# Kernel tuning notes

Measured on AMD Instinct MI355X. Metric: run time of the kernel, lower is better.

## Reference

```python
import jax, jax.numpy as jnp
import numpy as np

B, S, T = 32, 128, 64
H = 512
VS = VT = 32000


def _lstm_cell(x, h, c, W, U, b):
    # Keras LSTM gate order: i, f, g(cell), o
    z = x @ W + h @ U + b
    i, f, g, o = jnp.split(z, 4, axis=-1)
    c = jax.nn.sigmoid(f) * c + jax.nn.sigmoid(i) * jnp.tanh(g)
    h = jax.nn.sigmoid(o) * jnp.tanh(c)
    return h, c


def _lstm_scan(xs, h0, c0, W, U, b):
    # xs: [S, B, D]
    def step(carry, x):
        h, c = _lstm_cell(x, carry[0], carry[1], W, U, b)
        return (h, c), h
    (hT, cT), hs = jax.lax.scan(step, (h0, c0), xs)
    return hs, hT, cT


def setup_inputs() -> dict:
    key = jax.random.key(0)
    ks = jax.random.split(key, 16)
    def n(k, shape, s=0.02):
        return (jax.random.normal(k, shape, jnp.float32) * s).astype(jnp.float32)
    return {
        "src": jax.random.randint(ks[0], (B, S), 0, VS, jnp.int32),
        "trg": jax.random.randint(ks[1], (B, T), 0, VT, jnp.int32),
        "E_src": n(ks[2], (VS, H)),
        "E_trg": n(ks[3], (VT, H)),
        "Wf": n(ks[4], (H, 4 * H)), "Uf": n(ks[5], (H, 4 * H)), "bf": jnp.zeros((4 * H,), jnp.float32),
        "Wb": n(ks[6], (H, 4 * H)), "Ub": n(ks[7], (H, 4 * H)), "bb": jnp.zeros((4 * H,), jnp.float32),
        "Wd": n(ks[8], (H, 4 * H)), "Ud": n(ks[9], (H, 4 * H)), "bd": jnp.zeros((4 * H,), jnp.float32),
        "fcW": n(ks[10], (2 * H, H)), "fcb": jnp.zeros((H,), jnp.float32),
        "clsW": n(ks[11], (2 * H, VT)), "clsb": jnp.zeros((VT,), jnp.float32),
    }


def reference(src, trg, E_src, E_trg, Wf, Uf, bf, Wb, Ub, bb, Wd, Ud, bd, fcW, fcb, clsW, clsb):
    Bn = src.shape[0]
    Hn = E_src.shape[1]
    # --- Encoder: bidirectional LSTM ---
    xs = E_src[src].transpose(1, 0, 2)          # [S, B, H]
    z0 = jnp.zeros((Bn, Hn), xs.dtype)
    hs_f, hf, cf = _lstm_scan(xs, z0, z0, Wf, Uf, bf)
    hs_b, hb, cb = _lstm_scan(xs[::-1], z0, z0, Wb, Ub, bb)
    src_hidden = jnp.concatenate([hs_f, hs_b[::-1]], axis=-1).transpose(1, 0, 2)  # [B, S, 2H]
    # --- shared fc projections (same Dense, 2H -> H) ---
    src_h = src_hidden @ fcW + fcb                                   # [B, S, H]
    prev_h = jnp.concatenate([hf, hb], axis=-1) @ fcW + fcb          # [B, H]
    prev_c = jnp.concatenate([cf, cb], axis=-1) @ fcW + fcb          # [B, H]
    neg = jnp.where(src == 0, jnp.float32(-1e9), jnp.float32(0.0))   # [B, S]
    # --- Decoder (teacher forcing): per-step LSTM cell + dot-product attention ---
    ys = E_trg[trg[:, :-1]].transpose(1, 0, 2)  # [T-1, B, H]

    def step(carry, x):
        h, c = _lstm_cell(x, carry[0], carry[1], Wd, Ud, bd)
        score = jnp.einsum('bh,bsh->bs', h, src_h) + neg
        attn = jax.nn.softmax(score, axis=-1)
        ws = jnp.einsum('bs,bsh->bh', attn, src_h)
        return (h, c), jnp.concatenate([ws, h], axis=-1)  # dec_state [B, 2H]

    _, dec = jax.lax.scan(step, (prev_h, prev_c), ys)     # [T-1, B, 2H]
    logits = dec.transpose(1, 0, 2) @ clsW + clsb          # [B, T-1, VT]
    return logits
```

## Files before the change

### kernel.cpp

```cpp
#include <hip/hip_runtime.h>
#include <hip/hip_bf16.h>
#include <stdint.h>
#include <string.h>

constexpr int cB = 32, cS = 128, cT = 64, cH = 512, cH4 = 2048, cVT = 32000, cTM1 = 63;

typedef __attribute__((ext_vector_type(8))) __bf16 bf16x8;
typedef __attribute__((ext_vector_type(4))) float f32x4;

__device__ __forceinline__ float sigm(float x) { return 1.0f / (1.0f + expf(-x)); }

__device__ __forceinline__ bf16x8 sc_load16(const __hip_bfloat16* p) {
  bf16x8 r;
  asm volatile("global_load_dwordx4 %0, %1, off sc0 sc1"
               : "=&v"(r) : "v"(p) : "memory");
  return r;
}
__device__ __forceinline__ void sc_store2(__hip_bfloat16* p, float hval) {
  __hip_bfloat16 hb = __float2bfloat16(hval);
  unsigned short us;
  memcpy(&us, &hb, 2);
  unsigned u = us;
  asm volatile("global_store_short %0, %1, off sc0 sc1"
               :: "v"(p), "v"(u) : "memory");
}

__device__ __forceinline__ void gridbar(unsigned* ctr, unsigned* flag,
                                        unsigned nblk, unsigned gen) {
  asm volatile("s_waitcnt vmcnt(0)" ::: "memory");
  __syncthreads();
  if (threadIdx.x == 0) {
    unsigned old = __hip_atomic_fetch_add(ctr, 1u, __ATOMIC_RELAXED,
                                          __HIP_MEMORY_SCOPE_AGENT);
    if (old == gen * nblk - 1u) {
      __hip_atomic_store(flag, gen, __ATOMIC_RELAXED, __HIP_MEMORY_SCOPE_AGENT);
    } else {
      while (__hip_atomic_load(flag, __ATOMIC_RELAXED, __HIP_MEMORY_SCOPE_AGENT) < gen)
        __builtin_amdgcn_s_sleep(1);
    }
  }
  __syncthreads();
}

__global__ __launch_bounds__(64) void k_init_bars(unsigned* p) {
  if (threadIdx.x < 16) p[threadIdx.x] = 0u;
}

__global__ __launch_bounds__(128) void k_embed_src(const int* __restrict__ src,
                                                   const float* __restrict__ E,
                                                   __hip_bfloat16* __restrict__ xs_bf,
                                                   float* __restrict__ neg) {
  int sb = blockIdx.x;
  int s = sb >> 5, b = sb & 31;
  int tok = src[b * cS + s];
  float4 e = ((const float4*)(E + (size_t)tok * cH))[threadIdx.x];
  __hip_bfloat16* drow = xs_bf + (size_t)sb * cH + threadIdx.x * 4;
  drow[0] = __float2bfloat16(e.x); drow[1] = __float2bfloat16(e.y);
  drow[2] = __float2bfloat16(e.z); drow[3] = __float2bfloat16(e.w);
  if (threadIdx.x == 0) neg[b * cS + s] = (tok == 0) ? -1e9f : 0.0f;
}

__global__ __launch_bounds__(128) void k_embed_trg(const int* __restrict__ trg,
                                                   const float* __restrict__ E,
                                                   __hip_bfloat16* __restrict__ ys_bf) {
  int tb = blockIdx.x;
  int t = tb >> 5, b = tb & 31;
  int tok = trg[b * cT + t];
  float4 e = ((const float4*)(E + (size_t)tok * cH))[threadIdx.x];
  __hip_bfloat16* drow = ys_bf + (size_t)tb * cH + threadIdx.x * 4;
  drow[0] = __float2bfloat16(e.x); drow[1] = __float2bfloat16(e.y);
  drow[2] = __float2bfloat16(e.z); drow[3] = __float2bfloat16(e.w);
}

__device__ __forceinline__ void f2bT_tile(const float* __restrict__ src,
                                          __hip_bfloat16* __restrict__ dst,
                                          int K, int N, int gi, int bx, int by,
                                          float (*t)[33]) {
  int nt = bx * 32, kt = by * 32;
  int c = threadIdx.x & 31, r0 = threadIdx.x >> 5;
#pragma unroll
  for (int i = 0; i < 4; ++i) {
    int r = r0 + i * 8;
    t[r][c] = src[(size_t)(kt + r) * N + nt + c];
  }
  __syncthreads();
#pragma unroll
  for (int i = 0; i < 4; ++i) {
    int row = nt + r0 + i * 8;
    int pr = gi ? (((row & 511) << 2) | (row >> 9)) : row;
    dst[(size_t)pr * K + kt + c] = __float2bfloat16(t[c][r0 + i * 8]);
  }
  __syncthreads();
}

__global__ __launch_bounds__(256) void k_prep(
    const float* __restrict__ Wf, const float* __restrict__ Wb, const float* __restrict__ Wd,
    const float* __restrict__ Uf, const float* __restrict__ Ub, const float* __restrict__ Ud,
    const float* __restrict__ fcW,
    const float* __restrict__ bf, const float* __restrict__ bb, const float* __restrict__ bd,
    __hip_bfloat16* __restrict__ Wtfx, __hip_bfloat16* __restrict__ Wtbx,
    __hip_bfloat16* __restrict__ Wtdx,
    __hip_bfloat16* __restrict__ Utf, __hip_bfloat16* __restrict__ Utb,
    __hip_bfloat16* __restrict__ Utd,
    __hip_bfloat16* __restrict__ fcWt,
    float* __restrict__ bfx, float* __restrict__ bbx, float* __restrict__ bdx,
    __hip_bfloat16* __restrict__ ys_pad) {
  __shared__ float t[32][33];
  int id = blockIdx.x;
  if (id < 6144) {
    int grp = id >> 10, r = id & 1023;
    const float* s; __hip_bfloat16* d;
    switch (grp) {
      case 0: s = Wf; d = Wtfx; break;
      case 1: s = Wb; d = Wtbx; break;
      case 2: s = Wd; d = Wtdx; break;
      case 3: s = Uf; d = Utf; break;
      case 4: s = Ub; d = Utb; break;
      default: s = Ud; d = Utd; break;
    }
    f2bT_tile(s, d, 512, 2048, 1, r & 63, r >> 6, t);
  } else if (id < 6656) {
    int r = id - 6144;
    f2bT_tile(fcW, fcWt, 1024, 512, 0, r & 15, r >> 4, t);
  } else if (id < 6680) {
    int r = id - 6656;
    const float* s = (r < 8) ? bf : ((r < 16) ? bb : bd);
    float* d = (r < 8) ? bfx : ((r < 16) ? bbx : bdx);
    int i = (r & 7) * 256 + threadIdx.x;
    d[i] = s[(i & 3) * 512 + (i >> 2)];
  } else {
    int r = id - 6680;
    ys_pad[r * 256 + threadIdx.x] = __float2bfloat16(0.0f);
  }
}

__global__ __launch_bounds__(256) void k_bgemm(const __hip_bfloat16* __restrict__ A,
                                               const __hip_bfloat16* __restrict__ Bt,
                                               const float* __restrict__ bias,
                                               float* __restrict__ C,
                                               int M, int K, int N) {
  __shared__ __hip_bfloat16 As[128 * 64];
  __shared__ __hip_bfloat16 Bs[128 * 64];
  const int tid = threadIdx.x;
  const int lane = tid & 63;
  const int wave = tid >> 6;
  const int wr = wave >> 1, wc = wave & 1;
  const int bm = blockIdx.x * 128, bn = blockIdx.y * 128;

  f32x4 acc[4][4] = {};

  const int srow = lane >> 3;
  const int scol = (lane & 7) * 8;

  for (int kt = 0; kt < K; kt += 64) {
#pragma unroll
    for (int i = 0; i < 4; ++i) {
      int c = wave * 4 + i;
      const __hip_bfloat16* ga = A + (size_t)(bm + c * 8 + srow) * K + kt + scol;
      __builtin_amdgcn_global_load_lds(
          (const __attribute__((address_space(1))) uint32_t*)ga,
          (__attribute__((address_space(3))) uint32_t*)(As + c * 512), 16, 0, 0);
      const __hip_bfloat16* gb = Bt + (size_t)(bn + c * 8 + srow) * K + kt + scol;
      __builtin_amdgcn_global_load_lds(
          (const __attribute__((address_space(1))) uint32_t*)gb,
          (__attribute__((address_space(3))) uint32_t*)(Bs + c * 512), 16, 0, 0);
    }
    __syncthreads();

#pragma unroll
    for (int kk = 0; kk < 64; kk += 32) {
      const int ko = kk + (lane >> 4) * 8;
      bf16x8 a[4], b[4];
      const int ar = wr * 64 + (lane & 15);
#pragma unroll
      for (int m = 0; m < 4; ++m)
        a[m] = *(const bf16x8*)(As + (size_t)(ar + m * 16) * 64 + ko);
      const int br = wc * 64 + (lane & 15);
#pragma unroll
      for (int n = 0; n < 4; ++n)
        b[n] = *(const bf16x8*)(Bs + (size_t)(br + n * 16) * 64 + ko);
#pragma unroll
      for (int m = 0; m < 4; ++m)
#pragma unroll
        for (int n = 0; n < 4; ++n)
          acc[m][n] = __builtin_amdgcn_mfma_f32_16x16x32_bf16(a[m], b[n], acc[m][n], 0, 0, 0);
    }
    __syncthreads();
  }

#pragma unroll
  for (int m = 0; m < 4; ++m) {
    const int row0 = bm + wr * 64 + m * 16 + (lane >> 4) * 4;
#pragma unroll
    for (int n = 0; n < 4; ++n) {
      const int col = bn + wc * 64 + n * 16 + (lane & 15);
      const float bv = bias[col];
#pragma unroll
      for (int r = 0; r < 4; ++r) {
        const int row = row0 + r;
        if (row < M) C[(size_t)row * N + col] = acc[m][n][r] + bv;
      }
    }
  }
}

__global__ __launch_bounds__(256, 1) void k_enc_mfma(
    const float* __restrict__ xWf, const float* __restrict__ xWb,
    const __hip_bfloat16* __restrict__ Utf, const __hip_bfloat16* __restrict__ Utb,
    __hip_bfloat16* __restrict__ hs_f, __hip_bfloat16* __restrict__ hs_b,
    __hip_bfloat16* __restrict__ henc,
    float* __restrict__ cf, float* __restrict__ cb,
    unsigned* bars) {
  const int bid = blockIdx.x;
  const int dir = bid >> 5, nb = bid & 31;
  const int c0 = nb * 64;
  const float* xW = dir ? xWb : xWf;
  const __hip_bfloat16* Ut = dir ? Utb : Utf;
  __hip_bfloat16* hs = dir ? hs_b : hs_f;
  __hip_bfloat16* hcur = henc + (size_t)dir * 32768;
  float* cOut = dir ? cb : cf;
  unsigned* ctr = bars + dir * 2;
  unsigned* flag = bars + dir * 2 + 1;

  __shared__ __hip_bfloat16 Hs[32][520];

  const int tid = threadIdx.x;
  const int lane = tid & 63;
  const int wv = tid >> 6;
  const int fr = lane & 15;
  const int fq = lane >> 4;

  bf16x8 afrag[16];
#pragma unroll
  for (int kk = 0; kk < 16; ++kk)
    afrag[kk] = *(const bf16x8*)(Ut + (size_t)(c0 + wv * 16 + fr) * 512 + kk * 32 + fq * 8);

  const int jglob = nb * 16 + wv * 4 + fq;
  const int b0 = fr, b1 = fr + 16;
  const int zc = c0 + wv * 16 + fq * 4;
  float cs0 = 0.f, cs1 = 0.f;

  const int trow0 = dir ? 127 : 0;
  float4 z0 = *(const float4*)(xW + ((size_t)(trow0 * 32 + b0)) * 2048 + zc);
  float4 z1 = *(const float4*)(xW + ((size_t)(trow0 * 32 + b1)) * 2048 + zc);

  for (int t = 0; t < 128; ++t) {
    const int trow = dir ? (127 - t) : t;
    if (t > 0) {
      const __hip_bfloat16* hsrc = hcur + (size_t)((t + 1) & 1) * 16384;
      bf16x8 hr[8];
#pragma unroll
      for (int i = 0; i < 8; ++i) {
        int c = tid + i * 256;
        hr[i] = sc_load16(hsrc + (size_t)c * 8);
      }
      asm volatile("s_waitcnt vmcnt(0)" ::: "memory");
      __builtin_amdgcn_sched_barrier(0);
#pragma unroll
      for (int i = 0; i < 8; ++i) {
        int c = tid + i * 256;
        int r = c >> 6, cc = (c & 63) * 8;
        *(bf16x8*)&Hs[r][cc] = hr[i];
      }
    }
    const int tn = (t < 127) ? t + 1 : 127;
    const int ntrow = dir ? (127 - tn) : tn;
    float4 zn0 = *(const float4*)(xW + ((size_t)(ntrow * 32 + b0)) * 2048 + zc);
    float4 zn1 = *(const float4*)(xW + ((size_t)(ntrow * 32 + b1)) * 2048 + zc);

    f32x4 acc0 = {}, acc1 = {};
    if (t > 0) {
      asm volatile("s_waitcnt lgkmcnt(0)" ::: "memory");
      __builtin_amdgcn_s_barrier();
      __builtin_amdgcn_sched_barrier(0);
#pragma unroll
      for (int kk = 0; kk < 16; ++kk) {
        bf16x8 h0v = *(const bf16x8*)&Hs[b0][kk * 32 + fq * 8];
        bf16x8 h1v = *(const bf16x8*)&Hs[b1][kk * 32 + fq * 8];
        acc0 = __builtin_amdgcn_mfma_f32_16x16x32_bf16(afrag[kk], h0v, acc0, 0, 0, 0);
        acc1 = __builtin_amdgcn_mfma_f32_16x16x32_bf16(afrag[kk], h1v, acc1, 0, 0, 0);
      }
    }
    {
      float zi = z0.x + acc0[0], zf = z0.y + acc0[1], zg = z0.z + acc0[2], zo = z0.w + acc0[3];
      cs0 = sigm(zf) * cs0 + sigm(zi) * tanhf(zg);
      float h = sigm(zo) * tanhf(cs0);
      sc_store2(hcur + (size_t)(t & 1) * 16384 + (size_t)b0 * 512 + jglob, h);
      hs[((size_t)trow * 32 + b0) * 512 + jglob] = __float2bfloat16(h);
    }
    {
      float zi = z1.x + acc1[0], zf = z1.y + acc1[1], zg = z1.z + acc1[2], zo = z1.w + acc1[3];
      cs1 = sigm(zf) * cs1 + sigm(zi) * tanhf(zg);
      float h = sigm(zo) * tanhf(cs1);
      sc_store2(hcur + (size_t)(t & 1) * 16384 + (size_t)b1 * 512 + jglob, h);
      hs[((size_t)trow * 32 + b1) * 512 + jglob] = __float2bfloat16(h);
    }
    z0 = zn0; z1 = zn1;
    if (t < 127) gridbar(ctr, flag, 32u, (unsigned)(t + 1));
  }
  cOut[(size_t)b0 * 512 + jglob] = cs0;
  cOut[(size_t)b1 * 512 + jglob] = cs1;
}

__global__ __launch_bounds__(256, 1) void k_dec_mfma(
    const float* __restrict__ yW, const __hip_bfloat16* __restrict__ Utd,
    const float* __restrict__ prev_h, const float* __restrict__ prev_c,
    __hip_bfloat16* __restrict__ hdec, __hip_bfloat16* __restrict__ decb,
    const float* __restrict__ clsW, __hip_bfloat16* __restrict__ clsWt,
    unsigned* ctr, unsigned* flag) {
  __shared__ __hip_bfloat16 Hs[32][520];
  __shared__ float tt[32][33];

  if (blockIdx.x >= 32) {
    for (int tile = blockIdx.x - 32; tile < 32000; tile += (int)gridDim.x - 32) {
      int bx = tile % 1000, by = tile / 1000;
      f2bT_tile(clsW, clsWt, 1024, 32000, 0, bx, by, tt);
    }
    return;
  }

  const int nb = blockIdx.x;
  const int c0 = nb * 64;
  const int tid = threadIdx.x;
  const int lane = tid & 63;
  const int wv = tid >> 6;
  const int fr = lane & 15;
  const int fq = lane >> 4;

  bf16x8 afrag[16];
#pragma unroll
  for (int kk = 0; kk < 16; ++kk)
    afrag[kk] = *(const bf16x8*)(Utd + (size_t)(c0 + wv * 16 + fr) * 512 + kk * 32 + fq * 8);

  const int jglob = nb * 16 + wv * 4 + fq;
  const int b0 = fr, b1 = fr + 16;
  const int zc = c0 + wv * 16 + fq * 4;
  float cs0 = prev_c[(size_t)b0 * 512 + jglob];
  float cs1 = prev_c[(size_t)b1 * 512 + jglob];

  float4 z0 = *(const float4*)(yW + ((size_t)b0) * 2048 + zc);
  float4 z1 = *(const float4*)(yW + ((size_t)b1) * 2048 + zc);

  for (int t = 0; t < cTM1; ++t) {
    if (t == 0) {
      const float4* ph4 = (const float4*)prev_h;
#pragma unroll
      for (int i = 0; i < 16; ++i) {
        int c = tid + i * 256;
        float4 v = ph4[c];
        int r = c >> 7, c4 = (c & 127) * 4;
        Hs[r][c4 + 0] = __float2bfloat16(v.x);
        Hs[r][c4 + 1] = __float2bfloat16(v.y);
        Hs[r][c4 + 2] = __float2bfloat16(v.z);
        Hs[r][c4 + 3] = __float2bfloat16(v.w);
      }
    } else {
      const __hip_bfloat16* hsrc = hdec + (size_t)((t + 1) & 1) * 16384;
      bf16x8 hr[8];
#pragma unroll
      for (int i = 0; i < 8; ++i) {
        int c = tid + i * 256;
        hr[i] = sc_load16(hsrc + (size_t)c * 8);
      }
      asm volatile("s_waitcnt vmcnt(0)" ::: "memory");
      __builtin_amdgcn_sched_barrier(0);
#pragma unroll
      for (int i = 0; i < 8; ++i) {
        int c = tid + i * 256;
        int r = c >> 6, cc = (c & 63) * 8;
        *(bf16x8*)&Hs[r][cc] = hr[i];
      }
    }
    const int tn = (t < cTM1 - 1) ? t + 1 : cTM1 - 1;
    float4 zn0 = *(const float4*)(yW + ((size_t)(tn * 32 + b0)) * 2048 + zc);
    float4 zn1 = *(const float4*)(yW + ((size_t)(tn * 32 + b1)) * 2048 + zc);

    asm volatile("s_waitcnt lgkmcnt(0)" ::: "memory");
    __builtin_amdgcn_s_barrier();
    __builtin_amdgcn_sched_barrier(0);

    f32x4 acc0 = {}, acc1 = {};
#pragma unroll
    for (int kk = 0; kk < 16; ++kk) {
      bf16x8 h0v = *(const bf16x8*)&Hs[b0][kk * 32 + fq * 8];
      bf16x8 h1v = *(const bf16x8*)&Hs[b1][kk * 32 + fq * 8];
      acc0 = __builtin_amdgcn_mfma_f32_16x16x32_bf16(afrag[kk], h0v, acc0, 0, 0, 0);
      acc1 = __builtin_amdgcn_mfma_f32_16x16x32_bf16(afrag[kk], h1v, acc1, 0, 0, 0);
    }
    {
      float zi = z0.x + acc0[0], zf = z0.y + acc0[1], zg = z0.z + acc0[2], zo = z0.w + acc0[3];
      cs0 = sigm(zf) * cs0 + sigm(zi) * tanhf(zg);
      float h = sigm(zo) * tanhf(cs0);
      sc_store2(hdec + (size_t)(t & 1) * 16384 + (size_t)b0 * 512 + jglob, h);
      decb[((size_t)b0 * cTM1 + t) * 1024 + 512 + jglob] = __float2bfloat16(h);
    }
    {
      float zi = z1.x + acc1[0], zf = z1.y + acc1[1], zg = z1.z + acc1[2], zo = z1.w + acc1[3];
      cs1 = sigm(zf) * cs1 + sigm(zi) * tanhf(zg);
      float h = sigm(zo) * tanhf(cs1);
      sc_store2(hdec + (size_t)(t & 1) * 16384 + (size_t)b1 * 512 + jglob, h);
      decb[((size_t)b1 * cTM1 + t) * 1024 + 512 + jglob] = __float2bfloat16(h);
    }
    z0 = zn0; z1 = zn1;
    if (t < cTM1 - 1) gridbar(ctr, flag, 32u, (unsigned)(t + 1));
  }
}

__global__ __launch_bounds__(128) void k_cat_bf(const __hip_bfloat16* __restrict__ hs_f,
                                                const __hip_bfloat16* __restrict__ hs_b,
                                                const float* __restrict__ cf,
                                                const float* __restrict__ cb,
                                                __hip_bfloat16* __restrict__ cat) {
  int r = blockIdx.x;
  int tid = threadIdx.x;
  __hip_bfloat16* drow = cat + (size_t)r * 1024 + tid * 8;
  if (r >= 4160) {
    bf16x8 zv = {};
    *(bf16x8*)drow = zv;
    return;
  }
  if (r < 4128) {
    const __hip_bfloat16 *pf, *pb;
    if (r < 4096) {
      int b = r >> 7, s = r & 127;
      pf = hs_f + ((size_t)s * 32 + b) * 512;
      pb = hs_b + ((size_t)s * 32 + b) * 512;
    } else {
      int b = r - 4096;
      pf = hs_f + ((size_t)127 * 32 + b) * 512;
      pb = hs_b + ((size_t)b) * 512;
    }
    const __hip_bfloat16* s8 = (tid < 64) ? (pf + tid * 8) : (pb + (tid - 64) * 8);
    *(bf16x8*)drow = *(const bf16x8*)s8;
  } else {
    int b = r - 4128;
    const float* s8 = (tid < 64) ? (cf + (size_t)b * 512 + tid * 8)
                                 : (cb + (size_t)b * 512 + (tid - 64) * 8);
    bf16x8 v;
#pragma unroll
    for (int i = 0; i < 8; ++i) v[i] = (__bf16)s8[i];
    *(bf16x8*)drow = v;
  }
}

__global__ __launch_bounds__(256) void k_attn_all(const float* __restrict__ src_h,
                                                  const float* __restrict__ neg,
                                                  __hip_bfloat16* __restrict__ decb) {
  int bid = blockIdx.x;
  int xcd = bid & 7, idx = bid >> 3;
  int b = xcd + 8 * (idx / 63);
  int t = idx % 63;
  int tx = threadIdx.x;
  __shared__ float hv[cH];
  __shared__ float part[256];
  __shared__ float sc[cS];
  __shared__ float red[cS];
  __hip_bfloat16* drow = decb + ((size_t)b * cTM1 + t) * (2 * cH);
  hv[tx] = __bfloat162float(drow[cH + tx]);
  hv[tx + 256] = __bfloat162float(drow[cH + tx + 256]);
  __syncthreads();
  {
    int s = tx >> 1, half = tx & 1;
    const float4* sr = (const float4*)(src_h + ((size_t)b * cS + s) * cH + half * 256);
    const float4* hh = (const float4*)(hv + half * 256);
    float acc = 0.f;
#pragma unroll 8
    for (int k = 0; k < 64; ++k) {
      float4 v = sr[k], h4 = hh[k];
      acc += v.x * h4.x + v.y * h4.y + v.z * h4.z + v.w * h4.w;
    }
    part[tx] = acc;
  }
  __syncthreads();
  if (tx < cS) {
    float s0 = part[2 * tx] + part[2 * tx + 1] + neg[b * cS + tx];
    sc[tx] = s0;
    red[tx] = s0;
  }
  __syncthreads();
  for (int off = 64; off >= 1; off >>= 1) {
    if (tx < off) red[tx] = fmaxf(red[tx], red[tx + off]);
    __syncthreads();
  }
  float mx = red[0];
  __syncthreads();
  float e = 0.f;
  if (tx < cS) { e = expf(sc[tx] - mx); red[tx] = e; }
  __syncthreads();
  for (int off = 64; off >= 1; off >>= 1) {
    if (tx < off) red[tx] += red[tx + off];
    __syncthreads();
  }
  float inv = 1.0f / red[0];
  __syncthreads();
  if (tx < cS) sc[tx] = e * inv;
  __syncthreads();
  float a0 = 0.f, a1 = 0.f;
  for (int s = 0; s < cS; ++s) {
    float w = sc[s];
    const float* sr = src_h + ((size_t)b * cS + s) * cH;
    a0 += w * sr[tx];
    a1 += w * sr[tx + 256];
  }
  drow[tx] = __float2bfloat16(a0);
  drow[tx + 256] = __float2bfloat16(a1);
}

extern "C" void kernel_launch(void* const* d_in, const int* in_sizes, int n_in,
                              void* d_out, int out_size, void* d_ws, size_t ws_size,
                              hipStream_t stream) {
  const int* src = (const int*)d_in[0];
  const int* trg = (const int*)d_in[1];
  const float* E_src = (const float*)d_in[2];
  const float* E_trg = (const float*)d_in[3];
  const float* Wf = (const float*)d_in[4];
  const float* Uf = (const float*)d_in[5];
  const float* bf = (const float*)d_in[6];
  const float* Wb = (const float*)d_in[7];
  const float* Ub = (const float*)d_in[8];
  const float* bb = (const float*)d_in[9];
  const float* Wd = (const float*)d_in[10];
  const float* Ud = (const float*)d_in[11];
  const float* bd = (const float*)d_in[12];
  const float* fcW = (const float*)d_in[13];
  const float* fcb = (const float*)d_in[14];
  const float* clsW = (const float*)d_in[15];
  const float* clsb = (const float*)d_in[16];
  float* out = (float*)d_out;
  float* ws = (float*)d_ws;

  float* xWf = ws;
  float* xWb = ws + 8388608;
  float* yW = ws + 16777216;
  __hip_bfloat16* hs_f = (__hip_bfloat16*)(ws + 20905984);
  __hip_bfloat16* hs_b = (__hip_bfloat16*)(ws + 21954560);
  float* cf = ws + 23003136;
  float* cb = ws + 23019520;
  float* neg = ws + 23035904;
  float* fco = ws + 23040000;
  __hip_bfloat16* decb = (__hip_bfloat16*)(ws + 25169920);
  __hip_bfloat16* Utd = (__hip_bfloat16*)(ws + 26218496);
  __hip_bfloat16* henc = (__hip_bfloat16*)(ws + 26742784);
  __hip_bfloat16* hdec = (__hip_bfloat16*)(ws + 26808320);
  unsigned* bars = (unsigned*)(ws + 26841088);
  float* pool = ws + 26841152;

  __hip_bfloat16* xs_bf = (__hip_bfloat16*)pool;
  __hip_bfloat16* ys_bf = (__hip_bfloat16*)(pool + 1048576);
  __hip_bfloat16* Utf = (__hip_bfloat16*)(pool + 1572864);
  __hip_bfloat16* Utb = (__hip_bfloat16*)(pool + 2097152);
  __hip_bfloat16* Wtfx = (__hip_bfloat16*)(pool + 2621440);
  __hip_bfloat16* Wtbx = (__hip_bfloat16*)(pool + 3145728);
  __hip_bfloat16* Wtdx = (__hip_bfloat16*)(pool + 3670016);
  float* bfx = pool + 4194304;
  float* bbx = pool + 4196352;
  float* bdx = pool + 4198400;
  __hip_bfloat16* fcWt = (__hip_bfloat16*)(pool + 4200448);
  __hip_bfloat16* cat_bf = (__hip_bfloat16*)pool;
  __hip_bfloat16* clsWt = (__hip_bfloat16*)xWf;

  k_embed_src<<<4096, 128, 0, stream>>>(src, E_src, xs_bf, neg);
  k_embed_trg<<<2016, 128, 0, stream>>>(trg, E_trg, ys_bf);
  k_prep<<<6744, 256, 0, stream>>>(Wf, Wb, Wd, Uf, Ub, Ud, fcW, bf, bb, bd,
                                   Wtfx, Wtbx, Wtdx, Utf, Utb, Utd, fcWt,
                                   bfx, bbx, bdx, ys_bf + (size_t)2016 * 512);

  k_bgemm<<<dim3(32, 16), 256, 0, stream>>>(xs_bf, Wtfx, bfx, xWf, 4096, 512, 2048);
  k_bgemm<<<dim3(32, 16), 256, 0, stream>>>(xs_bf, Wtbx, bbx, xWb, 4096, 512, 2048);
  k_bgemm<<<dim3(16, 16), 256, 0, stream>>>(ys_bf, Wtdx, bdx, yW, 2016, 512, 2048);

  k_init_bars<<<1, 64, 0, stream>>>(bars);
  k_enc_mfma<<<64, 256, 0, stream>>>(xWf, xWb, Utf, Utb, hs_f, hs_b, henc, cf, cb, bars);

  k_cat_bf<<<4224, 128, 0, stream>>>(hs_f, hs_b, cf, cb, cat_bf);
  k_bgemm<<<dim3(33, 4), 256, 0, stream>>>(cat_bf, fcWt, fcb, fco, 4160, 1024, 512);

  const float* prev_h = fco + (size_t)4096 * 512;
  const float* prev_c = fco + (size_t)4128 * 512;
  k_dec_mfma<<<256, 256, 0, stream>>>(yW, Utd, prev_h, prev_c, hdec, decb,
                                      clsW, clsWt, bars + 4, bars + 5);
  k_attn_all<<<2016, 256, 0, stream>>>(fco, neg, decb);

  k_bgemm<<<dim3(16, 250), 256, 0, stream>>>(decb, clsWt, clsb, out, 2016, 1024, 32000);
}
```

Baseline: 1.392 ms.

## Stage LSTM hidden outputs in LDS, use dword stores and leaner grid barrier

Each block now writes its new hidden values to a small LDS tile and then stores them as coalesced 4-byte stores, replacing scattered 2-byte stores to both the exchange buffer and the history buffer. The grid barrier no longer drains all outstanding memory ops; it waits with vmcnt(2) so the next step's gate prefetch can stay in flight across the barrier. The time loop is unrolled by two, with ping-pong prefetch registers instead of copies. The aim is a shorter per-step critical path in the sequential recurrence, at the cost of an extra LDS round trip and barrier, plus more delicate memory ordering around the grid sync.

```diff
diff --git a/kernel.cpp b/kernel.cpp
--- a/kernel.cpp
+++ b/kernel.cpp
@@ -16,19 +16,19 @@
                : "=&v"(r) : "v"(p) : "memory");
   return r;
 }
-__device__ __forceinline__ void sc_store2(__hip_bfloat16* p, float hval) {
-  __hip_bfloat16 hb = __float2bfloat16(hval);
-  unsigned short us;
-  memcpy(&us, &hb, 2);
-  unsigned u = us;
-  asm volatile("global_store_short %0, %1, off sc0 sc1"
-               :: "v"(p), "v"(u) : "memory");
-}
-
-__device__ __forceinline__ void gridbar(unsigned* ctr, unsigned* flag,
-                                        unsigned nblk, unsigned gen) {
-  asm volatile("s_waitcnt vmcnt(0)" ::: "memory");
-  __syncthreads();
+__device__ __forceinline__ void sc_store4(__hip_bfloat16* p, unsigned v) {
+  asm volatile("global_store_dword %0, %1, off sc0 sc1"
+               :: "v"(p), "v"(v) : "memory");
+}
+__device__ __forceinline__ void pl_store4(__hip_bfloat16* p, unsigned v) {
+  asm volatile("global_store_dword %0, %1, off"
+               :: "v"(p), "v"(v) : "memory");
+}
+
+__device__ __forceinline__ void gridbar_nw(unsigned* ctr, unsigned* flag,
+                                           unsigned nblk, unsigned gen) {
+  __builtin_amdgcn_sched_barrier(0);
+  __builtin_amdgcn_s_barrier();
   if (threadIdx.x == 0) {
     unsigned old = __hip_atomic_fetch_add(ctr, 1u, __ATOMIC_RELAXED,
                                           __HIP_MEMORY_SCOPE_AGENT);
@@ -39,7 +39,8 @@
         __builtin_amdgcn_s_sleep(1);
     }
   }
-  __syncthreads();
+  __builtin_amdgcn_s_barrier();
+  __builtin_amdgcn_sched_barrier(0);
 }
 
 __global__ __launch_bounds__(64) void k_init_bars(unsigned* p) {
@@ -204,6 +205,71 @@
   }
 }
 
+#define ENC_STEP(T, ZI0, ZI1, ZO0, ZO1)                                          \
+  {                                                                              \
+    const int t = (T);                                                           \
+    const int trow = dir ? (127 - t) : t;                                        \
+    if (t > 0) {                                                                 \
+      const __hip_bfloat16* hsrc = hcur + (size_t)((t + 1) & 1) * 16384;         \
+      bf16x8 hr[8];                                                              \
+      _Pragma("unroll")                                                          \
+      for (int i = 0; i < 8; ++i) {                                              \
+        int c = tid + i * 256;                                                   \
+        hr[i] = sc_load16(hsrc + (size_t)c * 8);                                 \
+      }                                                                          \
+      asm volatile("s_waitcnt vmcnt(0)" ::: "memory");                           \
+      __builtin_amdgcn_sched_barrier(0);                                         \
+      _Pragma("unroll")                                                          \
+      for (int i = 0; i < 8; ++i) {                                              \
+        int c = tid + i * 256;                                                   \
+        int r = c >> 6, cc = (c & 63) * 8;                                       \
+        *(bf16x8*)&Hs[r][cc] = hr[i];                                            \
+      }                                                                          \
+      asm volatile("s_waitcnt lgkmcnt(0)" ::: "memory");                         \
+      __builtin_amdgcn_s_barrier();                                              \
+      __builtin_amdgcn_sched_barrier(0);                                         \
+    }                                                                            \
+    f32x4 acc0 = {}, acc1 = {};                                                  \
+    if (t > 0) {                                                                 \
+      _Pragma("unroll")                                                          \
+      for (int kk = 0; kk < 16; ++kk) {                                          \
+        bf16x8 h0v = *(const bf16x8*)&Hs[b0][kk * 32 + fq * 8];                  \
+        bf16x8 h1v = *(const bf16x8*)&Hs[b1][kk * 32 + fq * 8];                  \
+        acc0 = __builtin_amdgcn_mfma_f32_16x16x32_bf16(afrag[kk], h0v, acc0, 0, 0, 0); \
+        acc1 = __builtin_amdgcn_mfma_f32_16x16x32_bf16(afrag[kk], h1v, acc1, 0, 0, 0); \
+      }                                                                          \
+    }                                                                            \
+    {                                                                            \
+      float zi = ZI0[0] + acc0[0], zf = ZI0[1] + acc0[1],                        \
+            zg = ZI0[2] + acc0[2], zo = ZI0[3] + acc0[3];                        \
+      cs0 = sigm(zf) * cs0 + sigm(zi) * tanhf(zg);                               \
+      Ho[b0][jloc] = __float2bfloat16(sigm(zo) * tanhf(cs0));                    \
+    }                                                                            \
+    {                                                                            \
+      float zi = ZI1[0] + acc1[0], zf = ZI1[1] + acc1[1],                        \
+            zg = ZI1[2] + acc1[2], zo = ZI1[3] + acc1[3];                        \
+      cs1 = sigm(zf) * cs1 + sigm(zi) * tanhf(zg);                               \
+      Ho[b1][jloc] = __float2bfloat16(sigm(zo) * tanhf(cs1));                    \
+    }                                                                            \
+    asm volatile("s_waitcnt lgkmcnt(0)" ::: "memory");                           \
+    __builtin_amdgcn_s_barrier();                                                \
+    __builtin_amdgcn_sched_barrier(0);                                           \
+    {                                                                            \
+      unsigned v = *(const unsigned*)&Ho[bb][jp];                                \
+      sc_store4(hcur + (size_t)(t & 1) * 16384 + (size_t)bb * 512 + nb * 16 + jp, v); \
+      pl_store4(hs + ((size_t)trow * 32 + bb) * 512 + nb * 16 + jp, v);          \
+    }                                                                            \
+    __builtin_amdgcn_sched_barrier(0);                                           \
+    const int tn = (t < 127) ? t + 1 : 127;                                      \
+    const int ntrow = dir ? (127 - tn) : tn;                                     \
+    ZO0 = *(const f32x4*)(xW + ((size_t)(ntrow * 32 + b0)) * 2048 + zc);         \
+    ZO1 = *(const f32x4*)(xW + ((size_t)(ntrow * 32 + b1)) * 2048 + zc);         \
+    if (t < 127) {                                                               \
+      asm volatile("s_waitcnt vmcnt(2)" ::: "memory");                           \
+      gridbar_nw(ctr, flag, 32u, (unsigned)(t + 1));                             \
+    }                                                                            \
+  }
+
 __global__ __launch_bounds__(256, 1) void k_enc_mfma(
     const float* __restrict__ xWf, const float* __restrict__ xWb,
     const __hip_bfloat16* __restrict__ Utf, const __hip_bfloat16* __restrict__ Utb,
@@ -223,6 +289,7 @@
   unsigned* flag = bars + dir * 2 + 1;
 
   __shared__ __hip_bfloat16 Hs[32][520];
+  __shared__ __hip_bfloat16 Ho[32][20];
 
   const int tid = threadIdx.x;
   const int lane = tid & 63;
@@ -236,71 +303,97 @@
     afrag[kk] = *(const bf16x8*)(Ut + (size_t)(c0 + wv * 16 + fr) * 512 + kk * 32 + fq * 8);
 
   const int jglob = nb * 16 + wv * 4 + fq;
+  const int jloc = wv * 4 + fq;
   const int b0 = fr, b1 = fr + 16;
   const int zc = c0 + wv * 16 + fq * 4;
+  const int bb = tid >> 3, jp = (tid & 7) * 2;
   float cs0 = 0.f, cs1 = 0.f;
 
   const int trow0 = dir ? 127 : 0;
-  float4 z0 = *(const float4*)(xW + ((size_t)(trow0 * 32 + b0)) * 2048 + zc);
-  float4 z1 = *(const float4*)(xW + ((size_t)(trow0 * 32 + b1)) * 2048 + zc);
-
-  for (int t = 0; t < 128; ++t) {
-    const int trow = dir ? (127 - t) : t;
-    if (t > 0) {
-      const __hip_bfloat16* hsrc = hcur + (size_t)((t + 1) & 1) * 16384;
-      bf16x8 hr[8];
-#pragma unroll
-      for (int i = 0; i < 8; ++i) {
-        int c = tid + i * 256;
-        hr[i] = sc_load16(hsrc + (size_t)c * 8);
-      }
-      asm volatile("s_waitcnt vmcnt(0)" ::: "memory");
-      __builtin_amdgcn_sched_barrier(0);
-#pragma unroll
-      for (int i = 0; i < 8; ++i) {
-        int c = tid + i * 256;
-        int r = c >> 6, cc = (c & 63) * 8;
-        *(bf16x8*)&Hs[r][cc] = hr[i];
-      }
-    }
-    const int tn = (t < 127) ? t + 1 : 127;
-    const int ntrow = dir ? (127 - tn) : tn;
-    float4 zn0 = *(const float4*)(xW + ((size_t)(ntrow * 32 + b0)) * 2048 + zc);
-    float4 zn1 = *(const float4*)(xW + ((size_t)(ntrow * 32 + b1)) * 2048 + zc);
-
-    f32x4 acc0 = {}, acc1 = {};
-    if (t > 0) {
-      asm volatile("s_waitcnt lgkmcnt(0)" ::: "memory");
-      __builtin_amdgcn_s_barrier();
-      __builtin_amdgcn_sched_barrier(0);
-#pragma unroll
-      for (int kk = 0; kk < 16; ++kk) {
-        bf16x8 h0v = *(const bf16x8*)&Hs[b0][kk * 32 + fq * 8];
-        bf16x8 h1v = *(const bf16x8*)&Hs[b1][kk * 32 + fq * 8];
-        acc0 = __builtin_amdgcn_mfma_f32_16x16x32_bf16(afrag[kk], h0v, acc0, 0, 0, 0);
-        acc1 = __builtin_amdgcn_mfma_f32_16x16x32_bf16(afrag[kk], h1v, acc1, 0, 0, 0);
-      }
-    }
-    {
-      float zi = z0.x + acc0[0], zf = z0.y + acc0[1], zg = z0.z + acc0[2], zo = z0.w + acc0[3];
-      cs0 = sigm(zf) * cs0 + sigm(zi) * tanhf(zg);
-      float h = sigm(zo) * tanhf(cs0);
-      sc_store2(hcur + (size_t)(t & 1) * 16384 + (size_t)b0 * 512 + jglob, h);
-      hs[((size_t)trow * 32 + b0) * 512 + jglob] = __float2bfloat16(h);
-    }
-    {
-      float zi = z1.x + acc1[0], zf = z1.y + acc1[1], zg = z1.z + acc1[2], zo = z1.w + acc1[3];
-      cs1 = sigm(zf) * cs1 + sigm(zi) * tanhf(zg);
-      float h = sigm(zo) * tanhf(cs1);
-      sc_store2(hcur + (size_t)(t & 1) * 16384 + (size_t)b1 * 512 + jglob, h);
-      hs[((size_t)trow * 32 + b1) * 512 + jglob] = __float2bfloat16(h);
-    }
-    z0 = zn0; z1 = zn1;
-    if (t < 127) gridbar(ctr, flag, 32u, (unsigned)(t + 1));
+  f32x4 zA0 = *(const f32x4*)(xW + ((size_t)(trow0 * 32 + b0)) * 2048 + zc);
+  f32x4 zA1 = *(const f32x4*)(xW + ((size_t)(trow0 * 32 + b1)) * 2048 + zc);
+  f32x4 zB0, zB1;
+
+  for (int it = 0; it < 64; ++it) {
+    ENC_STEP(2 * it, zA0, zA1, zB0, zB1);
+    ENC_STEP(2 * it + 1, zB0, zB1, zA0, zA1);
   }
   cOut[(size_t)b0 * 512 + jglob] = cs0;
   cOut[(size_t)b1 * 512 + jglob] = cs1;
 }
+
+#define DEC_STEP(T, ZI0, ZI1, ZO0, ZO1)                                          \
+  {                                                                              \
+    const int t = (T);                                                           \
+    if (t == 0) {                                                                \
+      const float4* ph4 = (const float4*)prev_h;                                 \
+      _Pragma("unroll")                                                          \
+      for (int i = 0; i < 16; ++i) {                                             \
+        int c = tid + i * 256;                                                   \
+        float4 v = ph4[c];                                                       \
+        int r = c >> 7, c4 = (c & 127) * 4;                                      \
+        Hs[r][c4 + 0] = __float2bfloat16(v.x);                                   \
+        Hs[r][c4 + 1] = __float2bfloat16(v.y);                                   \
+        Hs[r][c4 + 2] = __float2bfloat16(v.z);                                   \
+        Hs[r][c4 + 3] = __float2bfloat16(v.w);                                   \
+      }                                                                          \
+    } else {                                                                     \
+      const __hip_bfloat16* hsrc = hdec + (size_t)((t + 1) & 1) * 16384;         \
+      bf16x8 hr[8];                                                              \
+      _Pragma("unroll")                                                          \
+      for (int i = 0; i < 8; ++i) {                                              \
+        int c = tid + i * 256;                                                   \
+        hr[i] = sc_load16(hsrc + (size_t)c * 8);                                 \
+      }                                                                          \
+      asm volatile("s_waitcnt vmcnt(0)" ::: "memory");                           \
+      __builtin_amdgcn_sched_barrier(0);                                         \
+      _Pragma("unroll")                                                          \
+      for (int i = 0; i < 8; ++i) {                                              \
+        int c = tid + i * 256;                                                   \
+        int r = c >> 6, cc = (c & 63) * 8;                                       \
+        *(bf16x8*)&Hs[r][cc] = hr[i];                                            \
+      }                                                                          \
+    }                                                                            \
+    asm volatile("s_waitcnt lgkmcnt(0)" ::: "memory");                           \
+    __builtin_amdgcn_s_barrier();                                                \
+    __builtin_amdgcn_sched_barrier(0);                                           \
+    f32x4 acc0 = {}, acc1 = {};                                                  \
+    _Pragma("unroll")                                                            \
+    for (int kk = 0; kk < 16; ++kk) {                                            \
+      bf16x8 h0v = *(const bf16x8*)&Hs[b0][kk * 32 + fq * 8];                    \
+      bf16x8 h1v = *(const bf16x8*)&Hs[b1][kk * 32 + fq * 8];                    \
+      acc0 = __builtin_amdgcn_mfma_f32_16x16x32_bf16(afrag[kk], h0v, acc0, 0, 0, 0); \
+      acc1 = __builtin_amdgcn_mfma_f32_16x16x32_bf16(afrag[kk], h1v, acc1, 0, 0, 0); \
+    }                                                                            \
+    {                                                                            \
+      float zi = ZI0[0] + acc0[0], zf = ZI0[1] + acc0[1],                        \
+            zg = ZI0[2] + acc0[2], zo = ZI0[3] + acc0[3];                        \
+      cs0 = sigm(zf) * cs0 + sigm(zi) * tanhf(zg);                               \
+      Ho[b0][jloc] = __float2bfloat16(sigm(zo) * tanhf(cs0));                    \
+    }                                                                            \
+    {                                                                            \
+      float zi = ZI1[0] + acc1[0], zf = ZI1[1] + acc1[1],                        \
+            zg = ZI1[2] + acc1[2], zo = ZI1[3] + acc1[3];                        \
+      cs1 = sigm(zf) * cs1 + sigm(zi) * tanhf(zg);                               \
+      Ho[b1][jloc] = __float2bfloat16(sigm(zo) * tanhf(cs1));                    \
+    }                                                                            \
+    asm volatile("s_waitcnt lgkmcnt(0)" ::: "memory");                           \
+    __builtin_amdgcn_s_barrier();                                                \
+    __builtin_amdgcn_sched_barrier(0);                                           \
+    {                                                                            \
+      unsigned v = *(const unsigned*)&Ho[bb][jp];                                \
+      sc_store4(hdec + (size_t)(t & 1) * 16384 + (size_t)bb * 512 + nb * 16 + jp, v); \
+      pl_store4(decb + ((size_t)bb * cTM1 + t) * 1024 + 512 + nb * 16 + jp, v);  \
+    }                                                                            \
+    __builtin_amdgcn_sched_barrier(0);                                           \
+    const int tn = (t < cTM1 - 1) ? t + 1 : cTM1 - 1;                            \
+    ZO0 = *(const f32x4*)(yW + ((size_t)(tn * 32 + b0)) * 2048 + zc);            \
+    ZO1 = *(const f32x4*)(yW + ((size_t)(tn * 32 + b1)) * 2048 + zc);            \
+    if (t < cTM1 - 1) {                                                          \
+      asm volatile("s_waitcnt vmcnt(2)" ::: "memory");                           \
+      gridbar_nw(ctr, flag, 32u, (unsigned)(t + 1));                             \
+    }                                                                            \
+  }
 
 __global__ __launch_bounds__(256, 1) void k_dec_mfma(
     const float* __restrict__ yW, const __hip_bfloat16* __restrict__ Utd,
@@ -309,12 +402,13 @@
     const float* __restrict__ clsW, __hip_bfloat16* __restrict__ clsWt,
     unsigned* ctr, unsigned* flag) {
   __shared__ __hip_bfloat16 Hs[32][520];
-  __shared__ float tt[32][33];
+  __shared__ __hip_bfloat16 Ho[32][20];
+  __shared__ float tcv[32][33];
 
   if (blockIdx.x >= 32) {
     for (int tile = blockIdx.x - 32; tile < 32000; tile += (int)gridDim.x - 32) {
       int bx = tile % 1000, by = tile / 1000;
-      f2bT_tile(clsW, clsWt, 1024, 32000, 0, bx, by, tt);
+      f2bT_tile(clsW, clsWt, 1024, 32000, 0, bx, by, tcv);
     }
     return;
   }
@@ -333,77 +427,22 @@
     afrag[kk] = *(const bf16x8*)(Utd + (size_t)(c0 + wv * 16 + fr) * 512 + kk * 32 + fq * 8);
 
   const int jglob = nb * 16 + wv * 4 + fq;
+  const int jloc = wv * 4 + fq;
   const int b0 = fr, b1 = fr + 16;
   const int zc = c0 + wv * 16 + fq * 4;
+  const int bb = tid >> 3, jp = (tid & 7) * 2;
   float cs0 = prev_c[(size_t)b0 * 512 + jglob];
   float cs1 = prev_c[(size_t)b1 * 512 + jglob];
 
-  float4 z0 = *(const float4*)(yW + ((size_t)b0) * 2048 + zc);
-  float4 z1 = *(const float4*)(yW + ((size_t)b1) * 2048 + zc);
-
-  for (int t = 0; t < cTM1; ++t) {
-    if (t == 0) {
-      const float4* ph4 = (const float4*)prev_h;
-#pragma unroll
-      for (int i = 0; i < 16; ++i) {
-        int c = tid + i * 256;
-        float4 v = ph4[c];
-        int r = c >> 7, c4 = (c & 127) * 4;
-        Hs[r][c4 + 0] = __float2bfloat16(v.x);
-        Hs[r][c4 + 1] = __float2bfloat16(v.y);
-        Hs[r][c4 + 2] = __float2bfloat16(v.z);
-        Hs[r][c4 + 3] = __float2bfloat16(v.w);
-      }
-    } else {
-      const __hip_bfloat16* hsrc = hdec + (size_t)((t + 1) & 1) * 16384;
-      bf16x8 hr[8];
-#pragma unroll
-      for (int i = 0; i < 8; ++i) {
-        int c = tid + i * 256;
-        hr[i] = sc_load16(hsrc + (size_t)c * 8);
-      }
-      asm volatile("s_waitcnt vmcnt(0)" ::: "memory");
-      __builtin_amdgcn_sched_barrier(0);
-#pragma unroll
-      for (int i = 0; i < 8; ++i) {
-        int c = tid + i * 256;
-        int r = c >> 6, cc = (c & 63) * 8;
-        *(bf16x8*)&Hs[r][cc] = hr[i];
-      }
-    }
-    const int tn = (t < cTM1 - 1) ? t + 1 : cTM1 - 1;
-    float4 zn0 = *(const float4*)(yW + ((size_t)(tn * 32 + b0)) * 2048 + zc);
-    float4 zn1 = *(const float4*)(yW + ((size_t)(tn * 32 + b1)) * 2048 + zc);
-
-    asm volatile("s_waitcnt lgkmcnt(0)" ::: "memory");
-    __builtin_amdgcn_s_barrier();
-    __builtin_amdgcn_sched_barrier(0);
-
-    f32x4 acc0 = {}, acc1 = {};
-#pragma unroll
-    for (int kk = 0; kk < 16; ++kk) {
-      bf16x8 h0v = *(const bf16x8*)&Hs[b0][kk * 32 + fq * 8];
-      bf16x8 h1v = *(const bf16x8*)&Hs[b1][kk * 32 + fq * 8];
-      acc0 = __builtin_amdgcn_mfma_f32_16x16x32_bf16(afrag[kk], h0v, acc0, 0, 0, 0);
-      acc1 = __builtin_amdgcn_mfma_f32_16x16x32_bf16(afrag[kk], h1v, acc1, 0, 0, 0);
-    }
-    {
-      float zi = z0.x + acc0[0], zf = z0.y + acc0[1], zg = z0.z + acc0[2], zo = z0.w + acc0[3];
-      cs0 = sigm(zf) * cs0 + sigm(zi) * tanhf(zg);
-      float h = sigm(zo) * tanhf(cs0);
-      sc_store2(hdec + (size_t)(t & 1) * 16384 + (size_t)b0 * 512 + jglob, h);
-      decb[((size_t)b0 * cTM1 + t) * 1024 + 512 + jglob] = __float2bfloat16(h);
-    }
-    {
-      float zi = z1.x + acc1[0], zf = z1.y + acc1[1], zg = z1.z + acc1[2], zo = z1.w + acc1[3];
-      cs1 = sigm(zf) * cs1 + sigm(zi) * tanhf(zg);
-      float h = sigm(zo) * tanhf(cs1);
-      sc_store2(hdec + (size_t)(t & 1) * 16384 + (size_t)b1 * 512 + jglob, h);
-      decb[((size_t)b1 * cTM1 + t) * 1024 + 512 + jglob] = __float2bfloat16(h);
-    }
-    z0 = zn0; z1 = zn1;
-    if (t < cTM1 - 1) gridbar(ctr, flag, 32u, (unsigned)(t + 1));
-  }
+  f32x4 zA0 = *(const f32x4*)(yW + ((size_t)b0) * 2048 + zc);
+  f32x4 zA1 = *(const f32x4*)(yW + ((size_t)b1) * 2048 + zc);
+  f32x4 zB0, zB1;
+
+  for (int it = 0; it < 31; ++it) {
+    DEC_STEP(2 * it, zA0, zA1, zB0, zB1);
+    DEC_STEP(2 * it + 1, zB0, zB1, zA0, zA1);
+  }
+  DEC_STEP(62, zA0, zA1, zB0, zB1);
 }
 
 __global__ __launch_bounds__(128) void k_cat_bf(const __hip_bfloat16* __restrict__ hs_f,
```

Result: faster. 1.243 ms (-10.7%).
